# Optimization experiments

Measured on AMD Instinct MI355X. Metric: run time of the kernel, lower is better.

Reference implementation:

```python
import jax, jax.numpy as jnp
import numpy as np

N, E, G, B, L = 24576, 98304, 512, 512, 1000
F_IN, H1, C1, C2, HID = 5, 2, 64, 128, 256


def setup_inputs() -> dict:
    key = jax.random.key(0)
    ks = jax.random.split(key, 20)
    rn = lambda k, s: jax.random.normal(k, s, jnp.float32) * 0.1
    return {
        "x": jax.random.normal(ks[0], (N, F_IN), jnp.float32),
        "edge_index": jax.random.randint(ks[1], (2, E), 0, N),
        "batch": jnp.sort(jax.random.randint(ks[2], (N,), 0, G)),
        "protein_seq": jax.random.randint(ks[3], (B, L), 0, 22),
        "W1": rn(ks[4], (F_IN, H1 * C1)), "att_src1": rn(ks[5], (H1, C1)), "att_dst1": rn(ks[6], (H1, C1)), "b1": jnp.zeros((H1 * C1,), jnp.float32),
        "W2": rn(ks[7], (H1 * C1, C2)), "att_src2": rn(ks[8], (1, C2)), "att_dst2": rn(ks[9], (1, C2)), "b2": jnp.zeros((C2,), jnp.float32),
        "Wd": rn(ks[10], (C2, HID)), "bd": jnp.zeros((HID,), jnp.float32),
        "Pe": rn(ks[11], (22, 64)),
        "K1": rn(ks[12], (64, 64, 3)), "bk1": jnp.zeros((64,), jnp.float32),
        "K2": rn(ks[13], (128, 64, 5)), "bk2": jnp.zeros((128,), jnp.float32),
        "Wp": rn(ks[14], (128, HID)), "bp": jnp.zeros((HID,), jnp.float32),
        "Wf1": rn(ks[15], (2 * HID, 128)), "bf1": jnp.zeros((128,), jnp.float32),
        "Wf2": rn(ks[16], (128, 64)), "bf2": jnp.zeros((64,), jnp.float32),
        "Wo": rn(ks[17], (64, 1)), "bo": jnp.zeros((1,), jnp.float32),
    }


def _gat(x, edge_index, W, att_src, att_dst, b, heads, out_ch):
    """PyG GATConv: add self-loops, per-edge LeakyReLU(0.2) scores, segment softmax over dst."""
    n = x.shape[0]
    h = (x @ W).reshape(n, heads, out_ch)
    loop = jnp.arange(n)
    src = jnp.concatenate([edge_index[0], loop])
    dst = jnp.concatenate([edge_index[1], loop])
    a_s = jnp.sum(h * att_src[None], axis=-1)  # [n, H]
    a_d = jnp.sum(h * att_dst[None], axis=-1)
    e = jax.nn.leaky_relu(a_s[src] + a_d[dst], negative_slope=0.2)  # [E+n, H]
    m = jax.ops.segment_max(e, dst, num_segments=n)
    w = jnp.exp(e - m[dst])
    den = jax.ops.segment_sum(w, dst, num_segments=n)
    alpha = w / (den[dst] + 1e-16)
    out = jax.ops.segment_sum(h[src] * alpha[..., None], dst, num_segments=n)
    return out.reshape(n, heads * out_ch) + b


def _conv1d(x, k, pad):  # x: [B,C,L], k: [O,I,K]
    return jax.lax.conv_general_dilated(x, k, (1,), [(pad, pad)], dimension_numbers=("NCH", "OIH", "NCH"))


def reference(x, edge_index, batch, protein_seq, W1, att_src1, att_dst1, b1, W2, att_src2, att_dst2, b2, Wd, bd, Pe, K1, bk1, K2, bk2, Wp, bp, Wf1, bf1, Wf2, bf2, Wo, bo):
    # drug branch (GAT x2 + global mean pool)
    g = jax.nn.elu(_gat(x, edge_index, W1, att_src1, att_dst1, b1, H1, C1))
    g = jax.nn.elu(_gat(g, edge_index, W2, att_src2, att_dst2, b2, 1, C2))
    sums = jax.ops.segment_sum(g, batch, num_segments=G)
    cnt = jax.ops.segment_sum(jnp.ones((g.shape[0], 1), g.dtype), batch, num_segments=G)
    drug = jax.nn.relu(sums / jnp.maximum(cnt, 1.0) @ Wd + bd)
    # protein branch (embed -> conv1d x2 -> global max pool)
    pe = Pe[protein_seq].transpose(0, 2, 1)  # [B, 64, L]
    p = jax.nn.elu(_conv1d(pe, K1, 1) + bk1[None, :, None])
    p = jax.nn.elu(_conv1d(p, K2, 2) + bk2[None, :, None])
    prot = jax.nn.relu(jnp.max(p, axis=2) @ Wp + bp)
    # head
    h = jnp.concatenate([drug, prot], axis=1)
    h = jax.nn.relu(h @ Wf1 + bf1)
    h = jax.nn.relu(h @ Wf2 + bf2)
    return h @ Wo + bo
```

## Files before the change

kernel.cpp:

```cpp
#include <hip/hip_runtime.h>
#include <hip/hip_bf16.h>
#include <math.h>

#define NN 24576
#define NE 98304
#define ETOT (NE + NN)
#define NG 512
#define NB 512
#define LL 1000
#define TL 60
#define NTILE 17
#define PROT_BLKS (NB * NTILE)
#define CNT_BLKS (ETOT / 256)
#define AS1_BLKS (NN * 2 / 256)

typedef __attribute__((ext_vector_type(8))) short short8;
typedef __attribute__((ext_vector_type(4))) short short4v;
typedef __attribute__((ext_vector_type(4))) float f32x4;

__device__ inline short f2bf(float x) {
    union { __hip_bfloat16 b; short s; } u;
    u.b = __float2bfloat16(x);
    return u.s;
}

__device__ inline float bf2f(short s) {
    return __uint_as_float(((unsigned)(unsigned short)s) << 16);
}

__global__ void k_init_prep(int* deg, int* cursor, float* sums, float* cnt,
                            const float* K1, const float* K2, const float* W2, const float* Pe,
                            const float* W1, const float* as1c, const float* ad1c,
                            const float* as2c, const float* ad2c, const float* bk1,
                            short* Bswz2, short* Bh2, short* Bl2, float* M1,
                            float* wvec) {
    int bid = blockIdx.x, t = threadIdx.x;
    if (bid < 256) {
        int i = bid * 256 + t;
        if (i < NN) { deg[i] = 0; cursor[i] = 0; }
        if (i < NG * 128) sums[i] = 0.f;
        if (i < NG) cnt[i] = 0.f;
        return;
    }
    int idx = (bid - 256) * 256 + t;
    if (idx < 20) {
        int q = idx % 10, hd = q / 5, f = q % 5;
        const float* av = (idx < 10) ? as1c : ad1c;
        float s = 0.f;
        for (int c = 0; c < 64; c++) s += W1[f * 128 + hd * 64 + c] * av[hd * 64 + c];
        wvec[idx < 10 ? q : 10 + q] = s;
    }
    if (idx >= 32 && idx < 288) {
        int q = idx - 32;
        int kk = q & 127;
        const float* av = (q < 128) ? as2c : ad2c;
        float s = 0.f;
        for (int n2 = 0; n2 < 128; n2++) s += W2[kk * 128 + n2] * av[n2];
        wvec[idx] = s;
    }
    if (idx < 22 * 3 * 64) {
        int tok = idx / 192, r2 = idx % 192;
        int k = r2 >> 6, oc = r2 & 63;
        float s = (k == 1) ? bk1[oc] : 0.f;
        for (int ic = 0; ic < 64; ic++) s += K1[oc * 192 + ic * 3 + k] * Pe[tok * 64 + ic];
        M1[idx] = s;
    }
    if (idx < 320 * 128) {
        int j = idx & 7, lane = (idx >> 3) & 63, rest = idx >> 9;
        int nt = rest & 7, kb = rest >> 3;
        int k = kb * 32 + ((lane >> 4) << 3) + j;
        int n = nt * 16 + (lane & 15);
        int kk = k / 64, i = k % 64;
        Bswz2[idx] = f2bf(K2[n * 320 + i * 5 + kk]);
    }
    if (idx < 128 * 128) {
        int j = idx & 7, lane = (idx >> 3) & 63, rest = idx >> 9;
        int nt = rest & 7, kb = rest >> 3;
        int k = kb * 32 + ((lane >> 4) << 3) + j;
        int n = nt * 16 + (lane & 15);
        float v = W2[k * 128 + n];
        short hh = f2bf(v);
        Bh2[idx] = hh;
        Bl2[idx] = f2bf(v - bf2f(hh));
    }
}

#define SSTR 72
__global__ __launch_bounds__(256, 6) void k_prot_cnt_as1(
    const int* seq, const float* M1,
    const short* Bswz2, float* pmaxp,
    const int* ei, int* deg, const int* batch, float* cnt,
    const float* x, const float* wvec, float* rec) {
    int bid = blockIdx.x;
    int t = threadIdx.x;

    if (bid < CNT_BLKS) {
        int e = bid * 256 + t;
        int d = (e < NE) ? ei[NE + e] : e - NE;
        atomicAdd(&deg[d], 1);
        return;
    }
    if (bid < CNT_BLKS + AS1_BLKS) {
        int idx = (bid - CNT_BLKS) * 256 + t;
        int n = idx >> 1, hd = idx & 1;
        float xv[5];
        float s = 0.f, dv = 0.f;
#pragma unroll
        for (int f = 0; f < 5; f++) {
            xv[f] = x[n * 5 + f];
            s += xv[f] * wvec[hd * 5 + f];
            dv += xv[f] * wvec[10 + hd * 5 + f];
        }
        float* rr = &rec[n * 16];
        if (hd == 0) {
#pragma unroll
            for (int f = 0; f < 5; f++) rr[f] = xv[f];
            rr[5] = s; rr[7] = dv;
            atomicAdd(&cnt[batch[n]], 1.f);
        } else {
            rr[6] = s; rr[8] = dv;
        }
        return;
    }

    __shared__ __align__(16) short s1[68 * SSTR];

    int pb = bid - (CNT_BLKS + AS1_BLKS);
    int b = pb / NTILE;
    int tile = pb - b * NTILE;
    int t0 = tile * TL;

    if (t < 36) {
        *(short8*)&s1[64 * SSTR + t * 8] = (short8){0, 0, 0, 0, 0, 0, 0, 0};
    }

    {
        int q = t >> 2, c0 = (t & 3) << 4;
        int l = t0 - 2 + q;
        short tmp[16];
        if (l >= 0 && l < LL) {
            float v[16];
#pragma unroll
            for (int j = 0; j < 16; j++) v[j] = 0.f;
#pragma unroll
            for (int k = 0; k < 3; k++) {
                int lp = l - 1 + k;
                if (lp >= 0 && lp < LL) {
                    int tok = seq[b * LL + lp];
                    const float4* mr = (const float4*)&M1[tok * 192 + k * 64 + c0];
#pragma unroll
                    for (int j = 0; j < 4; j++) {
                        float4 mv = mr[j];
                        v[j * 4 + 0] += mv.x; v[j * 4 + 1] += mv.y;
                        v[j * 4 + 2] += mv.z; v[j * 4 + 3] += mv.w;
                    }
                }
            }
#pragma unroll
            for (int j = 0; j < 16; j++) {
                float xv = v[j];
                xv = xv > 0.f ? xv : __expf(xv) - 1.f;
                tmp[j] = f2bf(xv);
            }
        } else {
#pragma unroll
            for (int j = 0; j < 16; j++) tmp[j] = 0;
        }
        *(short8*)&s1[q * SSTR + c0] = *(short8*)&tmp[0];
        *(short8*)&s1[q * SSTR + c0 + 8] = *(short8*)&tmp[8];
    }
    __syncthreads();

    int wv = t >> 6, lane = t & 63;
    int ln15 = lane & 15, quad = lane >> 4;

    f32x4 acc2[4][2];
#pragma unroll
    for (int mi = 0; mi < 4; mi++)
#pragma unroll
        for (int ni = 0; ni < 2; ni++) acc2[mi][ni] = (f32x4){0.f, 0.f, 0.f, 0.f};
#pragma unroll
    for (int kb = 0; kb < 10; kb++) {
        int koff = kb * 32 + quad * 8;
        int kk = koff >> 6, i0 = koff & 63;
        short8 a[4], bb[2];
#pragma unroll
        for (int mi = 0; mi < 4; mi++)
            a[mi] = *(const short8*)&s1[(mi * 16 + ln15 + kk) * SSTR + i0];
#pragma unroll
        for (int ni = 0; ni < 2; ni++)
            bb[ni] = *(const short8*)&Bswz2[((kb * 8 + wv * 2 + ni) * 64 + lane) * 8];
#pragma unroll
        for (int mi = 0; mi < 4; mi++)
#pragma unroll
            for (int ni = 0; ni < 2; ni++)
                acc2[mi][ni] = __builtin_amdgcn_mfma_f32_16x16x32_bf16(a[mi], bb[ni], acc2[mi][ni], 0, 0, 0);
    }

#pragma unroll
    for (int ni = 0; ni < 2; ni++) {
        int col = (wv * 2 + ni) * 16 + ln15;
        float mx = -1e30f;
#pragma unroll
        for (int mi = 0; mi < 4; mi++) {
#pragma unroll
            for (int r = 0; r < 4; r++) {
                int p = mi * 16 + quad * 4 + r;
                if (p < TL && t0 + p < LL) mx = fmaxf(mx, acc2[mi][ni][r]);
            }
        }
        mx = fmaxf(mx, __shfl_xor(mx, 16, 64));
        mx = fmaxf(mx, __shfl_xor(mx, 32, 64));
        if (quad == 0) pmaxp[(b * NTILE + tile) * 128 + col] = mx;
    }
}

__global__ void k_scan1(const int* deg, int* excl, int* part) {
    __shared__ int s[256];
    int b = blockIdx.x, t = threadIdx.x, i = b * 256 + t;
    int v = deg[i];
    s[t] = v;
    __syncthreads();
    for (int o = 1; o < 256; o <<= 1) {
        int x = (t >= o) ? s[t - o] : 0;
        __syncthreads();
        s[t] += x;
        __syncthreads();
    }
    excl[i] = s[t] - v;
    if (t == 255) part[b] = s[t];
}

__global__ void k_scan23(const int* excl, const int* part, int* rowptr) {
    __shared__ int sp[96];
    __shared__ int pref;
    int b = blockIdx.x, t = threadIdx.x;
    if (t < 96) sp[t] = part[t];
    __syncthreads();
    if (t == 0) {
        int run = 0;
        for (int i = 0; i < b; i++) run += sp[i];
        pref = run;
    }
    __syncthreads();
    int i = b * 256 + t;
    rowptr[i] = excl[i] + pref;
    if (i == 0) rowptr[NN] = ETOT;
}

__global__ void k_scatter(const int* ei, const int* rowptr, int* cursor, int* colidx) {
    int e = blockIdx.x * 256 + threadIdx.x;
    if (e >= ETOT) return;
    int s, d;
    if (e < NE) { s = ei[e]; d = ei[NE + e]; }
    else { s = d = e - NE; }
    int pos = atomicAdd(&cursor[d], 1);
    colidx[rowptr[d] + pos] = s;
}

__global__ void k_agg2x(const int* rowptr, const int* colidx, const float* rec,
                        const float* W1, const float* b1, const float* wvec,
                        unsigned int* g1b, float* as2, float* ad2) {
    __shared__ float sW[640];
    __shared__ float sb1[128];
    __shared__ float swa[256];
    int t = threadIdx.x;
    for (int i = t; i < 640; i += 256) sW[i] = W1[i];
    if (t < 128) { sb1[t] = b1[t]; swa[t] = wvec[32 + t]; swa[128 + t] = wvec[160 + t]; }
    __syncthreads();

    int d = blockIdx.x * 16 + (t >> 4);
    int g = t & 15;
    int hd = (g < 5) ? 0 : 1;
    int f = (g < 5) ? g : g - 5;
    float adv = rec[d * 16 + 7 + hd];
    int p0 = rowptr[d], p1 = rowptr[d + 1];
    float den = 0.f, acc = 0.f;
    if (g < 10) {
        for (int pc = p0; pc < p1; pc += 4) {
            int sarr[4]; float ev[4], xv[4];
#pragma unroll
            for (int i = 0; i < 4; i++) {
                int pp = pc + i;
                sarr[i] = colidx[pp < p1 ? pp : p1 - 1];
            }
#pragma unroll
            for (int i = 0; i < 4; i++) {
                ev[i] = rec[sarr[i] * 16 + 5 + hd];
                xv[i] = rec[sarr[i] * 16 + f];
            }
#pragma unroll
            for (int i = 0; i < 4; i++) {
                if (pc + i < p1) {
                    float e = ev[i] + adv;
                    e = e >= 0.f ? e : 0.2f * e;
                    float w = __expf(e);
                    den += w;
                    acc += w * xv[i];
                }
            }
        }
    }
    float xn = acc / (den + 1e-16f);
    int gb = (t & 63) & ~15;
    int hcol = g >> 3;
    float xs[5];
#pragma unroll
    for (int f2 = 0; f2 < 5; f2++)
        xs[f2] = __shfl(xn, gb + hcol * 5 + f2, 64);
    float ps = 0.f, pd = 0.f;
    float g1v[8];
#pragma unroll
    for (int k = 0; k < 8; k++) {
        int col = g * 8 + k;
        float v = sb1[col];
#pragma unroll
        for (int f2 = 0; f2 < 5; f2++) v += xs[f2] * sW[f2 * 128 + col];
        v = v > 0.f ? v : __expf(v) - 1.f;
        g1v[k] = v;
        ps += v * swa[col];
        pd += v * swa[128 + col];
    }
    uint4 pk;
    pk.x = ((unsigned)(unsigned short)f2bf(g1v[1]) << 16) | (unsigned)(unsigned short)f2bf(g1v[0]);
    pk.y = ((unsigned)(unsigned short)f2bf(g1v[3]) << 16) | (unsigned)(unsigned short)f2bf(g1v[2]);
    pk.z = ((unsigned)(unsigned short)f2bf(g1v[5]) << 16) | (unsigned)(unsigned short)f2bf(g1v[4]);
    pk.w = ((unsigned)(unsigned short)f2bf(g1v[7]) << 16) | (unsigned)(unsigned short)f2bf(g1v[6]);
    *(uint4*)&g1b[d * 64 + g * 4] = pk;
#pragma unroll
    for (int msk = 1; msk < 16; msk <<= 1) {
        ps += __shfl_xor(ps, msk, 64);
        pd += __shfl_xor(pd, msk, 64);
    }
    if (g == 0) { as2[d] = ps; ad2[d] = pd; }
}

__global__ void k_agg1y(const int* rowptr, const int* colidx, const unsigned int* hb,
                        const float* as_, const float* ad_, float* yacc) {
    int t = threadIdx.x;
    int d = blockIdx.x * 4 + (t >> 6);
    int c = t & 63;
    float adv = ad_[d];
    int p0 = rowptr[d], p1 = rowptr[d + 1];
    float den = 0.f, acc0 = 0.f, acc1 = 0.f;
    for (int pc = p0; pc < p1; pc += 4) {
        int sarr[4]; float ev[4]; unsigned int hv[4];
#pragma unroll
        for (int i = 0; i < 4; i++) {
            int pp = pc + i;
            sarr[i] = colidx[pp < p1 ? pp : p1 - 1];
        }
#pragma unroll
        for (int i = 0; i < 4; i++) {
            ev[i] = as_[sarr[i]];
            hv[i] = hb[sarr[i] * 64 + c];
        }
#pragma unroll
        for (int i = 0; i < 4; i++) {
            if (pc + i < p1) {
                float e = ev[i] + adv;
                e = e >= 0.f ? e : 0.2f * e;
                float w = __expf(e);
                den += w;
                acc0 += w * __uint_as_float(hv[i] << 16);
                acc1 += w * __uint_as_float(hv[i] & 0xFFFF0000u);
            }
        }
    }
    float inv = 1.f / (den + 1e-16f);
    ((float2*)yacc)[d * 64 + c] = (float2){acc0 * inv, acc1 * inv};
}

#define ASTR 136
__global__ __launch_bounds__(256, 2) void k_g2mm(
    const float* yacc, const short* Bh, const short* Bl, const float* b2,
    const int* batch, float* sums) {
    __shared__ __align__(16) short Ah[64 * ASTR];
    __shared__ __align__(16) short Al[64 * ASTR];
    __shared__ int sb[64];
    int t = threadIdx.x;
    int m0 = blockIdx.x * 64;
    int wv = t >> 6, lane = t & 63;
    int ln15 = lane & 15, quad = lane >> 4;

    if (t < 64) sb[t] = batch[m0 + t];
    for (int i = t; i < 64 * 32; i += 256) {
        int row = i >> 5, c4 = (i & 31) * 4;
        float4 v = *(const float4*)&yacc[(m0 + row) * 128 + c4];
        short4v hi, lo;
        hi.x = f2bf(v.x); lo.x = f2bf(v.x - bf2f(hi.x));
        hi.y = f2bf(v.y); lo.y = f2bf(v.y - bf2f(hi.y));
        hi.z = f2bf(v.z); lo.z = f2bf(v.z - bf2f(hi.z));
        hi.w = f2bf(v.w); lo.w = f2bf(v.w - bf2f(hi.w));
        *(short4v*)&Ah[row * ASTR + c4] = hi;
        *(short4v*)&Al[row * ASTR + c4] = lo;
    }
    __syncthreads();

    f32x4 acc[8];
#pragma unroll
    for (int nt = 0; nt < 8; nt++) acc[nt] = (f32x4){0.f, 0.f, 0.f, 0.f};
    int arow = wv * 16 + ln15;
#pragma unroll
    for (int kb = 0; kb < 4; kb++) {
        int koff = kb * 32 + quad * 8;
        short8 a_hi = *(const short8*)&Ah[arow * ASTR + koff];
        short8 a_lo = *(const short8*)&Al[arow * ASTR + koff];
#pragma unroll
        for (int nt = 0; nt < 8; nt++) {
            short8 bh = *(const short8*)&Bh[((kb * 8 + nt) * 64 + lane) * 8];
            short8 bl = *(const short8*)&Bl[((kb * 8 + nt) * 64 + lane) * 8];
            acc[nt] = __builtin_amdgcn_mfma_f32_16x16x32_bf16(a_hi, bh, acc[nt], 0, 0, 0);
            acc[nt] = __builtin_amdgcn_mfma_f32_16x16x32_bf16(a_hi, bl, acc[nt], 0, 0, 0);
            acc[nt] = __builtin_amdgcn_mfma_f32_16x16x32_bf16(a_lo, bh, acc[nt], 0, 0, 0);
        }
    }
    int rbase = wv * 16 + quad * 4;
#pragma unroll
    for (int nt = 0; nt < 8; nt++) {
        int col = nt * 16 + ln15;
        float bias = b2[col];
        float run = 0.f;
        int cg = sb[rbase];
#pragma unroll
        for (int r = 0; r < 4; r++) {
            float v = acc[nt][r] + bias;
            v = v > 0.f ? v : __expf(v) - 1.f;
            int g = sb[rbase + r];
            if (g != cg) {
                atomicAdd(&sums[cg * 128 + col], run);
                run = 0.f; cg = g;
            }
            run += v;
        }
        atomicAdd(&sums[cg * 128 + col], run);
    }
}

__global__ __launch_bounds__(512) void k_tail(
    const float* pmaxp, const float* bk2, const float* Wp, const float* bp,
    const float* sums, const float* cnt, const float* Wd, const float* bd,
    const float* Wf1, const float* bf1, const float* Wf2, const float* bf2,
    const float* Wo, const float* bo, float* out) {
    __shared__ float spm[128];
    __shared__ float in2[512];
    __shared__ float part1[512];
    __shared__ float hh[128];
    __shared__ float part2[512];
    __shared__ float h2s[64];
    int g = blockIdx.x, t = threadIdx.x;

    if (t < 128) {
        float m = -1e30f;
#pragma unroll
        for (int tt = 0; tt < NTILE; tt++)
            m = fmaxf(m, pmaxp[(g * NTILE + tt) * 128 + t]);
        float v = m + bk2[t];
        spm[t] = v > 0.f ? v : __expf(v) - 1.f;
    }
    __syncthreads();

    if (t < 256) {
        float pacc = bp[t];
#pragma unroll 8
        for (int i = 0; i < 128; i++) pacc += spm[i] * Wp[i * 256 + t];
        in2[256 + t] = pacc > 0.f ? pacc : 0.f;
    } else {
        int o = t - 256;
        float c = cnt[g]; c = c < 1.f ? 1.f : c;
        float inv = 1.f / c;
        float dacc = bd[o];
#pragma unroll 8
        for (int i = 0; i < 128; i++) dacc += sums[g * 128 + i] * inv * Wd[i * 256 + o];
        in2[o] = dacc > 0.f ? dacc : 0.f;
    }
    __syncthreads();

    {
        int o = t >> 2, ks = t & 3;
        float p = 0.f;
        int c0 = ks * 128;
#pragma unroll 8
        for (int cc = c0; cc < c0 + 128; cc++) p += in2[cc] * Wf1[cc * 128 + o];
        part1[t] = p;
    }
    __syncthreads();
    if (t < 128) {
        float a = bf1[t] + part1[t * 4] + part1[t * 4 + 1] + part1[t * 4 + 2] + part1[t * 4 + 3];
        hh[t] = a > 0.f ? a : 0.f;
    }
    __syncthreads();

    {
        int o = t >> 3, ks = t & 7;
        float p = 0.f;
        int c0 = ks * 16;
#pragma unroll
        for (int cc = c0; cc < c0 + 16; cc++) p += hh[cc] * Wf2[cc * 64 + o];
        part2[t] = p;
    }
    __syncthreads();
    if (t < 64) {
        float a = bf2[t];
#pragma unroll
        for (int k = 0; k < 8; k++) a += part2[t * 8 + k];
        h2s[t] = a > 0.f ? a : 0.f;
    }
    __syncthreads();

    if (t < 64) {
        float p = h2s[t] * Wo[t];
#pragma unroll
        for (int off = 32; off > 0; off >>= 1) p += __shfl_down(p, off, 64);
        if (t == 0) out[g] = p + bo[0];
    }
}

extern "C" void kernel_launch(void* const* d_in, const int* in_sizes, int n_in,
                              void* d_out, int out_size, void* d_ws, size_t ws_size,
                              hipStream_t stream) {
    (void)in_sizes; (void)n_in; (void)out_size; (void)ws_size;
    const float* x   = (const float*)d_in[0];
    const int* ei    = (const int*)d_in[1];
    const int* batch = (const int*)d_in[2];
    const int* seq   = (const int*)d_in[3];
    const float* W1  = (const float*)d_in[4];
    const float* a_s1 = (const float*)d_in[5];
    const float* a_d1 = (const float*)d_in[6];
    const float* b1  = (const float*)d_in[7];
    const float* W2  = (const float*)d_in[8];
    const float* a_s2 = (const float*)d_in[9];
    const float* a_d2 = (const float*)d_in[10];
    const float* b2  = (const float*)d_in[11];
    const float* Wd  = (const float*)d_in[12];
    const float* bd  = (const float*)d_in[13];
    const float* Pe  = (const float*)d_in[14];
    const float* K1  = (const float*)d_in[15];
    const float* bk1 = (const float*)d_in[16];
    const float* K2  = (const float*)d_in[17];
    const float* bk2 = (const float*)d_in[18];
    const float* Wp  = (const float*)d_in[19];
    const float* bp  = (const float*)d_in[20];
    const float* Wf1 = (const float*)d_in[21];
    const float* bf1 = (const float*)d_in[22];
    const float* Wf2 = (const float*)d_in[23];
    const float* bf2 = (const float*)d_in[24];
    const float* Wo  = (const float*)d_in[25];
    const float* bo  = (const float*)d_in[26];
    float* out = (float*)d_out;

    float* w = (float*)d_ws;
    float* g1bf = w; w += NN * 64;
    float* yacc = w; w += NN * 128;
    float* as2  = w; w += NN;
    float* ad2  = w; w += NN;
    float* sums = w; w += NG * 128;
    float* cnt  = w; w += NG;
    float* pmaxp = w; w += NB * NTILE * 128;
    float* rec  = w; w += NN * 16;
    float* wvec = w; w += 512;
    short* Bswz2 = (short*)w; w += 320 * 128 / 2;
    short* Bh2  = (short*)w; w += 128 * 128 / 2;
    short* Bl2  = (short*)w; w += 128 * 128 / 2;
    float* M1   = w; w += 22 * 3 * 64;
    int* deg    = (int*)w; w += NN;
    int* cursor = (int*)w; w += NN;
    int* excl   = (int*)w; w += NN;
    int* part   = (int*)w; w += 128;
    int* rowptr = (int*)w; w += NN + 8;
    int* colidx = (int*)w; w += ETOT;

    unsigned int* g1b = (unsigned int*)g1bf;

    hipLaunchKernelGGL(k_init_prep, dim3(256 + 160), dim3(256), 0, stream,
                       deg, cursor, sums, cnt,
                       K1, K2, W2, Pe, W1, a_s1, a_d1, a_s2, a_d2, bk1,
                       Bswz2, Bh2, Bl2, M1, wvec);

    hipLaunchKernelGGL(k_prot_cnt_as1, dim3(CNT_BLKS + AS1_BLKS + PROT_BLKS), dim3(256), 0, stream,
                       seq, M1, Bswz2, pmaxp,
                       ei, deg, batch, cnt, x, wvec, rec);

    hipLaunchKernelGGL(k_scan1, dim3(NN / 256), dim3(256), 0, stream, deg, excl, part);
    hipLaunchKernelGGL(k_scan23, dim3(NN / 256), dim3(256), 0, stream, excl, part, rowptr);
    hipLaunchKernelGGL(k_scatter, dim3(ETOT / 256), dim3(256), 0, stream, ei, rowptr, cursor, colidx);

    hipLaunchKernelGGL(k_agg2x, dim3(NN / 16), dim3(256), 0, stream,
                       rowptr, colidx, rec, W1, b1, wvec, g1b, as2, ad2);

    hipLaunchKernelGGL(k_agg1y, dim3(NN / 4), dim3(256), 0, stream,
                       rowptr, colidx, g1b, as2, ad2, yacc);

    hipLaunchKernelGGL(k_g2mm, dim3(NN / 64), dim3(256), 0, stream,
                       yacc, Bh2, Bl2, b2, batch, sums);

    hipLaunchKernelGGL(k_tail, dim3(NG), dim3(512), 0, stream,
                       pmaxp, bk2, Wp, bp, sums, cnt, Wd, bd, Wf1, bf1, Wf2, bf2, Wo, bo, out);
}
```

Baseline: 282.6 us.

## Merge scan kernels with atomic grid barrier and reorder fused protein/count blocks

```diff
diff --git a/kernel.cpp b/kernel.cpp
--- a/kernel.cpp
+++ b/kernel.cpp
@@ -28,10 +28,10 @@
     return __uint_as_float(((unsigned)(unsigned short)s) << 16);
 }
 
-__global__ void k_init_prep(int* deg, int* cursor, float* sums, float* cnt,
+__global__ void k_init_prep(int* deg, int* cursor, float* sums, float* cnt, int* ctr,
                             const float* K1, const float* K2, const float* W2, const float* Pe,
                             const float* W1, const float* as1c, const float* ad1c,
-                            const float* as2c, const float* ad2c, const float* bk1,
+                            const float* as2c, const float* ad2c,
                             short* Bswz2, short* Bh2, short* Bl2, float* M1,
                             float* wvec) {
     int bid = blockIdx.x, t = threadIdx.x;
@@ -40,6 +40,7 @@
         if (i < NN) { deg[i] = 0; cursor[i] = 0; }
         if (i < NG * 128) sums[i] = 0.f;
         if (i < NG) cnt[i] = 0.f;
+        if (i == 0) ctr[0] = 0;
         return;
     }
     int idx = (bid - 256) * 256 + t;
@@ -61,7 +62,7 @@
     if (idx < 22 * 3 * 64) {
         int tok = idx / 192, r2 = idx % 192;
         int k = r2 >> 6, oc = r2 & 63;
-        float s = (k == 1) ? bk1[oc] : 0.f;
+        float s = 0.f;
         for (int ic = 0; ic < 64; ic++) s += K1[oc * 192 + ic * 3 + k] * Pe[tok * 64 + ic];
         M1[idx] = s;
     }
@@ -87,47 +88,47 @@
 
 #define SSTR 72
 __global__ __launch_bounds__(256, 6) void k_prot_cnt_as1(
-    const int* seq, const float* M1,
+    const int* seq, const float* M1, const float* bk1,
     const short* Bswz2, float* pmaxp,
     const int* ei, int* deg, const int* batch, float* cnt,
     const float* x, const float* wvec, float* rec) {
     int bid = blockIdx.x;
     int t = threadIdx.x;
 
-    if (bid < CNT_BLKS) {
-        int e = bid * 256 + t;
-        int d = (e < NE) ? ei[NE + e] : e - NE;
-        atomicAdd(&deg[d], 1);
+    if (bid >= PROT_BLKS) {
+        int rb = bid - PROT_BLKS;
+        if (rb < CNT_BLKS) {
+            int e = rb * 256 + t;
+            int d = (e < NE) ? ei[NE + e] : e - NE;
+            atomicAdd(&deg[d], 1);
+        } else {
+            int idx = (rb - CNT_BLKS) * 256 + t;
+            int n = idx >> 1, hd = idx & 1;
+            float xv[5];
+            float s = 0.f, dv = 0.f;
+#pragma unroll
+            for (int f = 0; f < 5; f++) {
+                xv[f] = x[n * 5 + f];
+                s += xv[f] * wvec[hd * 5 + f];
+                dv += xv[f] * wvec[10 + hd * 5 + f];
+            }
+            float* rr = &rec[n * 16];
+            if (hd == 0) {
+#pragma unroll
+                for (int f = 0; f < 5; f++) rr[f] = xv[f];
+                rr[5] = s; rr[7] = dv;
+                atomicAdd(&cnt[batch[n]], 1.f);
+            } else {
+                rr[6] = s; rr[8] = dv;
+            }
+        }
         return;
     }
-    if (bid < CNT_BLKS + AS1_BLKS) {
-        int idx = (bid - CNT_BLKS) * 256 + t;
-        int n = idx >> 1, hd = idx & 1;
-        float xv[5];
-        float s = 0.f, dv = 0.f;
-#pragma unroll
-        for (int f = 0; f < 5; f++) {
-            xv[f] = x[n * 5 + f];
-            s += xv[f] * wvec[hd * 5 + f];
-            dv += xv[f] * wvec[10 + hd * 5 + f];
-        }
-        float* rr = &rec[n * 16];
-        if (hd == 0) {
-#pragma unroll
-            for (int f = 0; f < 5; f++) rr[f] = xv[f];
-            rr[5] = s; rr[7] = dv;
-            atomicAdd(&cnt[batch[n]], 1.f);
-        } else {
-            rr[6] = s; rr[8] = dv;
-        }
-        return;
-    }
 
     __shared__ __align__(16) short s1[68 * SSTR];
 
-    int pb = bid - (CNT_BLKS + AS1_BLKS);
-    int b = pb / NTILE;
-    int tile = pb - b * NTILE;
+    int b = bid / NTILE;
+    int tile = bid - b * NTILE;
     int t0 = tile * TL;
 
     if (t < 36) {
@@ -141,7 +142,10 @@
         if (l >= 0 && l < LL) {
             float v[16];
 #pragma unroll
-            for (int j = 0; j < 16; j++) v[j] = 0.f;
+            for (int j = 0; j < 4; j++) {
+                float4 bv = *(const float4*)&bk1[c0 + j * 4];
+                v[j * 4 + 0] = bv.x; v[j * 4 + 1] = bv.y; v[j * 4 + 2] = bv.z; v[j * 4 + 3] = bv.w;
+            }
 #pragma unroll
             for (int k = 0; k < 3; k++) {
                 int lp = l - 1 + k;
@@ -179,7 +183,7 @@
     for (int mi = 0; mi < 4; mi++)
 #pragma unroll
         for (int ni = 0; ni < 2; ni++) acc2[mi][ni] = (f32x4){0.f, 0.f, 0.f, 0.f};
-#pragma unroll
+#pragma unroll 2
     for (int kb = 0; kb < 10; kb++) {
         int koff = kb * 32 + quad * 8;
         int kk = koff >> 6, i0 = koff & 63;
@@ -215,36 +219,34 @@
     }
 }
 
-__global__ void k_scan1(const int* deg, int* excl, int* part) {
+__global__ void k_scan(const int* deg, int* rowptr, int* part, int* ctr) {
     __shared__ int s[256];
+    __shared__ int sp[96];
     int b = blockIdx.x, t = threadIdx.x, i = b * 256 + t;
     int v = deg[i];
     s[t] = v;
     __syncthreads();
     for (int o = 1; o < 256; o <<= 1) {
-        int x = (t >= o) ? s[t - o] : 0;
+        int x2 = (t >= o) ? s[t - o] : 0;
         __syncthreads();
-        s[t] += x;
+        s[t] += x2;
         __syncthreads();
     }
-    excl[i] = s[t] - v;
-    if (t == 255) part[b] = s[t];
-}
-
-__global__ void k_scan23(const int* excl, const int* part, int* rowptr) {
-    __shared__ int sp[96];
-    __shared__ int pref;
-    int b = blockIdx.x, t = threadIdx.x;
-    if (t < 96) sp[t] = part[t];
-    __syncthreads();
+    int excl = s[t] - v;
+    if (t == 255) {
+        part[b] = s[t];
+        __threadfence();
+        atomicAdd(ctr, 1);
+    }
     if (t == 0) {
-        int run = 0;
-        for (int i = 0; i < b; i++) run += sp[i];
-        pref = run;
-    }
-    __syncthreads();
-    int i = b * 256 + t;
-    rowptr[i] = excl[i] + pref;
+        while (__hip_atomic_load(ctr, __ATOMIC_ACQUIRE, __HIP_MEMORY_SCOPE_AGENT) < 96) {}
+    }
+    __syncthreads();
+    if (t < 96) sp[t] = __hip_atomic_load(&part[t], __ATOMIC_RELAXED, __HIP_MEMORY_SCOPE_AGENT);
+    __syncthreads();
+    int pref = 0;
+    for (int i2 = 0; i2 < b; i2++) pref += sp[i2];
+    rowptr[i] = excl + pref;
     if (i == 0) rowptr[NN] = ETOT;
 }
 
@@ -565,24 +567,24 @@
     float* M1   = w; w += 22 * 3 * 64;
     int* deg    = (int*)w; w += NN;
     int* cursor = (int*)w; w += NN;
-    int* excl   = (int*)w; w += NN;
     int* part   = (int*)w; w += 128;
+    int* ctr    = (int*)w; w += 8;
     int* rowptr = (int*)w; w += NN + 8;
     int* colidx = (int*)w; w += ETOT;
 
     unsigned int* g1b = (unsigned int*)g1bf;
 
     hipLaunchKernelGGL(k_init_prep, dim3(256 + 160), dim3(256), 0, stream,
-                       deg, cursor, sums, cnt,
-                       K1, K2, W2, Pe, W1, a_s1, a_d1, a_s2, a_d2, bk1,
+                       deg, cursor, sums, cnt, ctr,
+                       K1, K2, W2, Pe, W1, a_s1, a_d1, a_s2, a_d2,
                        Bswz2, Bh2, Bl2, M1, wvec);
 
-    hipLaunchKernelGGL(k_prot_cnt_as1, dim3(CNT_BLKS + AS1_BLKS + PROT_BLKS), dim3(256), 0, stream,
-                       seq, M1, Bswz2, pmaxp,
+    hipLaunchKernelGGL(k_prot_cnt_as1, dim3(PROT_BLKS + CNT_BLKS + AS1_BLKS), dim3(256), 0, stream,
+                       seq, M1, bk1, Bswz2, pmaxp,
                        ei, deg, batch, cnt, x, wvec, rec);
 
-    hipLaunchKernelGGL(k_scan1, dim3(NN / 256), dim3(256), 0, stream, deg, excl, part);
-    hipLaunchKernelGGL(k_scan23, dim3(NN / 256), dim3(256), 0, stream, excl, part, rowptr);
+    hipLaunchKernelGGL(k_scan, dim3(NN / 256), dim3(256), 0, stream, deg, rowptr, part, ctr);
+
     hipLaunchKernelGGL(k_scatter, dim3(ETOT / 256), dim3(256), 0, stream, ei, rowptr, cursor, colidx);
 
     hipLaunchKernelGGL(k_agg2x, dim3(NN / 16), dim3(256), 0, stream,
```

New measurement: 285.8 us. About the same (+1.1%).
